# Kernel optimization log

Hardware: AMD Instinct MI355X
Metric: run time of the kernel (lower is better)

The kernel has to match this reference:

```python
import jax, jax.numpy as jnp
import numpy as np

NEG_INF = -1e9  # matches masked_fill value -1000000000.0
SLOPE = 0.2     # LeakyReLU negative slope


def setup_inputs() -> dict:
    key = jax.random.key(0)
    k1, k2, k3, k4 = jax.random.split(key, 4)
    B, N, Fin, Fout = 16, 1024, 256, 256
    h = jax.random.normal(k1, (B, N, Fin), dtype=jnp.float32)
    adj = jax.random.randint(k2, (B, N, N), 0, 2, dtype=jnp.int32)
    W = jax.random.normal(k3, (Fin, Fout), dtype=jnp.float32) * (1.0 / np.sqrt(Fin))
    a = jax.random.normal(k4, (2 * Fout,), dtype=jnp.float32) * (1.0 / np.sqrt(2 * Fout))
    return {"h": h, "adj": adj, "W": W, "a": a}


def reference(h, adj, W, a):
    # h: [B,N,Fin], adj: [B,N,N] (0/1), W: [Fin,Fout], a: [2*Fout]
    Fout = W.shape[1]
    Wh = jnp.einsum("bnf,fo->bno", h, W)            # [B,N,Fout]
    a1, a2 = a[:Fout], a[Fout:]
    # e[b,i,j] = leakyrelu( Wh[b,i]·a1 + Wh[b,j]·a2 )  == a(cat(Wh_i, Wh_j))
    f1 = Wh @ a1                                     # [B,N]
    f2 = Wh @ a2                                     # [B,N]
    e = jax.nn.leaky_relu(f1[:, :, None] + f2[:, None, :], negative_slope=SLOPE)
    e = jnp.where(adj == 0, NEG_INF, e)              # mask non-edges
    attention = jax.nn.softmax(e, axis=-1)           # [B,N,N]
    # dropout is identity at eval / p=0
    h_prime = jnp.einsum("bij,bjo->bio", attention, Wh)  # [B,N,Fout]
    return h_prime
```

## Files before the change

### kernel.cpp

```cpp
#include <hip/hip_runtime.h>

typedef __attribute__((ext_vector_type(8))) short bf16x8;
typedef __attribute__((ext_vector_type(4))) float f32x4;

__device__ __forceinline__ unsigned short f2bf(float x) {
    unsigned int u = __float_as_uint(x);
    u += 0x7FFFu + ((u >> 16) & 1u);
    return (unsigned short)(u >> 16);
}

__device__ __forceinline__ void gl_lds16(const void* g, void* l) {
    __builtin_amdgcn_global_load_lds(
        (__attribute__((address_space(1))) void*)((void*)g),
        (__attribute__((address_space(3))) void*)l, 16, 0, 0);
}

__global__ __launch_bounds__(256) void prep(const float* __restrict__ W,
                                            short* __restrict__ WbT) {
    __shared__ float tile[32][33];
    const int t = threadIdx.x;
    const int bx = blockIdx.x & 7, by = blockIdx.x >> 3;
    const int r0 = by * 32, c0 = bx * 32;
    const int lr = t >> 5, lc = t & 31;
#pragma unroll
    for (int q = 0; q < 4; ++q)
        tile[q * 8 + lr][lc] = W[(r0 + q * 8 + lr) * 256 + c0 + lc];
    __syncthreads();
#pragma unroll
    for (int q = 0; q < 4; ++q)
        WbT[(c0 + q * 8 + lr) * 256 + r0 + lc] = (short)f2bf(tile[lc][q * 8 + lr]);
}

__global__ __launch_bounds__(256, 4) void wh_f12(const float* __restrict__ h,
                                                 const short* __restrict__ WbT,
                                                 const float* __restrict__ a,
                                                 short* __restrict__ WhT,
                                                 float* __restrict__ f1,
                                                 float* __restrict__ f2) {
    __shared__ short hA[32][264];
    __shared__ float sp[2][4][32];
    const int t = threadIdx.x;
    const int wid = t >> 6, lane = t & 63;
    const int quad = lane >> 4, l15 = lane & 15;
    const int m0 = blockIdx.x * 32;

#pragma unroll
    for (int rr = 0; rr < 2; ++rr) {
        const int r = rr * 16 + (t >> 4), c0 = (t & 15) * 16;
        const float* hp = h + (size_t)(m0 + r) * 256 + c0;
        float4 v0 = *(const float4*)(hp + 0), v1 = *(const float4*)(hp + 4);
        float4 v2 = *(const float4*)(hp + 8), v3 = *(const float4*)(hp + 12);
        bf16x8 w0, w1;
        w0[0] = (short)f2bf(v0.x); w0[1] = (short)f2bf(v0.y);
        w0[2] = (short)f2bf(v0.z); w0[3] = (short)f2bf(v0.w);
        w0[4] = (short)f2bf(v1.x); w0[5] = (short)f2bf(v1.y);
        w0[6] = (short)f2bf(v1.z); w0[7] = (short)f2bf(v1.w);
        w1[0] = (short)f2bf(v2.x); w1[1] = (short)f2bf(v2.y);
        w1[2] = (short)f2bf(v2.z); w1[3] = (short)f2bf(v2.w);
        w1[4] = (short)f2bf(v3.x); w1[5] = (short)f2bf(v3.y);
        w1[6] = (short)f2bf(v3.z); w1[7] = (short)f2bf(v3.w);
        *(bf16x8*)&hA[r][c0] = w0;
        *(bf16x8*)&hA[r][c0 + 8] = w1;
    }
    __syncthreads();

    f32x4 acc[2][4] = {};
#pragma unroll
    for (int kt = 0; kt < 8; ++kt) {
        const int k0 = kt * 32;
        bf16x8 bv[4];
#pragma unroll
        for (int ft = 0; ft < 4; ++ft)
            bv[ft] = *(const bf16x8*)(WbT + (size_t)(wid * 64 + ft * 16 + l15) * 256 + k0 + quad * 8);
        bf16x8 a0 = *(const bf16x8*)&hA[l15][k0 + quad * 8];
        bf16x8 a1 = *(const bf16x8*)&hA[16 + l15][k0 + quad * 8];
#pragma unroll
        for (int ft = 0; ft < 4; ++ft) {
            acc[0][ft] = __builtin_amdgcn_mfma_f32_16x16x32_bf16(a0, bv[ft], acc[0][ft], 0, 0, 0);
            acc[1][ft] = __builtin_amdgcn_mfma_f32_16x16x32_bf16(a1, bv[ft], acc[1][ft], 0, 0, 0);
        }
    }

    const int b = m0 >> 10;
#pragma unroll
    for (int mf = 0; mf < 2; ++mf) {
        const int il0 = (m0 & 1023) + mf * 16 + quad * 4;
#pragma unroll
        for (int ft = 0; ft < 4; ++ft) {
            const int f = wid * 64 + ft * 16 + l15;
            ushort4 pk;
            pk.x = f2bf(acc[mf][ft][0]);
            pk.y = f2bf(acc[mf][ft][1]);
            pk.z = f2bf(acc[mf][ft][2]);
            pk.w = f2bf(acc[mf][ft][3]);
            *(ushort4*)(WhT + ((size_t)b << 18) + (size_t)f * 1024 + il0) = pk;
        }
    }

    float a1v[4], a2v[4];
#pragma unroll
    for (int ft = 0; ft < 4; ++ft) {
        a1v[ft] = a[wid * 64 + ft * 16 + l15];
        a2v[ft] = a[256 + wid * 64 + ft * 16 + l15];
    }
    float p1[2][4] = {}, p2[2][4] = {};
#pragma unroll
    for (int mf = 0; mf < 2; ++mf)
#pragma unroll
        for (int ft = 0; ft < 4; ++ft)
#pragma unroll
            for (int r = 0; r < 4; ++r) {
                p1[mf][r] += acc[mf][ft][r] * a1v[ft];
                p2[mf][r] += acc[mf][ft][r] * a2v[ft];
            }
#pragma unroll
    for (int off = 1; off < 16; off <<= 1)
#pragma unroll
        for (int mf = 0; mf < 2; ++mf)
#pragma unroll
            for (int r = 0; r < 4; ++r) {
                p1[mf][r] += __shfl_xor(p1[mf][r], off);
                p2[mf][r] += __shfl_xor(p2[mf][r], off);
            }
    if (l15 == 0)
#pragma unroll
        for (int mf = 0; mf < 2; ++mf)
#pragma unroll
            for (int r = 0; r < 4; ++r) {
                sp[0][wid][mf * 16 + quad * 4 + r] = p1[mf][r];
                sp[1][wid][mf * 16 + quad * 4 + r] = p2[mf][r];
            }
    __syncthreads();
    if (t < 32) {
        f1[m0 + t] = sp[0][0][t] + sp[0][1][t] + sp[0][2][t] + sp[0][3][t];
        f2[m0 + t] = sp[1][0][t] + sp[1][1][t] + sp[1][2][t] + sp[1][3][t];
    }
}

__global__ __launch_bounds__(256) void stats_p(const int* __restrict__ adj,
                                               const float* __restrict__ f1g,
                                               const float* __restrict__ f2g,
                                               short* __restrict__ P) {
    const int wid = threadIdx.x >> 6, lane = threadIdx.x & 63;
    const int gid = blockIdx.x * 4 + wid;
    const int b = gid >> 10;
    const int* arow = adj + (size_t)gid * 1024;
    const float* f2b = f2g + (b << 10);
    const float f1r = f1g[gid];

    float e[16];
#pragma unroll
    for (int c = 0; c < 4; ++c) {
        int4 av = *(const int4*)(arow + lane * 4 + c * 256);
        float4 fv = *(const float4*)(f2b + lane * 4 + c * 256);
        float x0 = f1r + fv.x, x1 = f1r + fv.y, x2 = f1r + fv.z, x3 = f1r + fv.w;
        e[c * 4 + 0] = av.x ? fmaxf(x0, 0.2f * x0) : -3.0e38f;
        e[c * 4 + 1] = av.y ? fmaxf(x1, 0.2f * x1) : -3.0e38f;
        e[c * 4 + 2] = av.z ? fmaxf(x2, 0.2f * x2) : -3.0e38f;
        e[c * 4 + 3] = av.w ? fmaxf(x3, 0.2f * x3) : -3.0e38f;
    }
    float m = e[0];
#pragma unroll
    for (int q = 1; q < 16; ++q) m = fmaxf(m, e[q]);
#pragma unroll
    for (int off = 32; off; off >>= 1) m = fmaxf(m, __shfl_xor(m, off));

    float p[16];
    float l = 0.f;
#pragma unroll
    for (int q = 0; q < 16; ++q) { p[q] = __expf(e[q] - m); l += p[q]; }
#pragma unroll
    for (int off = 32; off; off >>= 1) l += __shfl_xor(l, off);
    const float invl = 1.0f / l;

    short* prow = P + (size_t)gid * 1024;
#pragma unroll
    for (int c = 0; c < 4; ++c) {
        ushort4 pk;
        pk.x = f2bf(p[c * 4 + 0] * invl);
        pk.y = f2bf(p[c * 4 + 1] * invl);
        pk.z = f2bf(p[c * 4 + 2] * invl);
        pk.w = f2bf(p[c * 4 + 3] * invl);
        *(ushort4*)(prow + lane * 4 + c * 256) = pk;
    }
}

__global__ __launch_bounds__(256, 4) void agg(const short* __restrict__ P,
                                              const short* __restrict__ WhT,
                                              float* __restrict__ out) {
    __shared__ short As[64 * 64];
    __shared__ short Bs[64 * 64];

    const int t = threadIdx.x;
    const int wid = t >> 6, lane = t & 63;
    const int quad = lane >> 4, l15 = lane & 15;
    const int m0 = blockIdx.x * 64, n0 = blockIdx.y * 64, b = blockIdx.z;

    const short* Pb = P + ((size_t)b << 20);
    const short* Wb = WhT + ((size_t)b << 18);

    const int r0 = t >> 3;
    const int w0 = (t & 7) ^ (r0 & 7);
    const short* gaA0 = Pb + (size_t)(m0 + r0) * 1024 + w0 * 8;
    const short* gaA1 = Pb + (size_t)(m0 + 32 + r0) * 1024 + w0 * 8;
    const short* gaB0 = Wb + (size_t)(n0 + r0) * 1024 + w0 * 8;
    const short* gaB1 = Wb + (size_t)(n0 + 32 + r0) * 1024 + w0 * 8;
    short* lA0 = As + t * 8;
    short* lA1 = As + 2048 + t * 8;
    short* lB0 = Bs + t * 8;
    short* lB1 = Bs + 2048 + t * 8;

    f32x4 acc[4] = {};
    const int ra = wid * 16 + l15;

    for (int k0 = 0; k0 < 1024; k0 += 64) {
        gl_lds16(gaA0 + k0, lA0);
        gl_lds16(gaA1 + k0, lA1);
        gl_lds16(gaB0 + k0, lB0);
        gl_lds16(gaB1 + k0, lB1);
        __syncthreads();

#pragma unroll
        for (int kt = 0; kt < 2; ++kt) {
            const int w = kt * 4 + quad;
            bf16x8 av = *(const bf16x8*)(As + ra * 64 + ((w ^ (ra & 7)) * 8));
#pragma unroll
            for (int nf = 0; nf < 4; ++nf) {
                const int rb = nf * 16 + l15;
                bf16x8 bv = *(const bf16x8*)(Bs + rb * 64 + ((w ^ (rb & 7)) * 8));
                acc[nf] = __builtin_amdgcn_mfma_f32_16x16x32_bf16(av, bv, acc[nf], 0, 0, 0);
            }
        }
        __syncthreads();
    }

    const int i = m0 + wid * 16 + quad * 4;
#pragma unroll
    for (int nf = 0; nf < 4; ++nf) {
        float* op = out + (size_t)((b << 10) + i) * 256 + n0 + nf * 16 + l15;
        op[0]   = acc[nf][0];
        op[256] = acc[nf][1];
        op[512] = acc[nf][2];
        op[768] = acc[nf][3];
    }
}

extern "C" void kernel_launch(void* const* d_in, const int* in_sizes, int n_in,
                              void* d_out, int out_size, void* d_ws, size_t ws_size,
                              hipStream_t stream) {
    const float* h   = (const float*)d_in[0];
    const int*   adj = (const int*)d_in[1];
    const float* W   = (const float*)d_in[2];
    const float* a   = (const float*)d_in[3];
    float* out = (float*)d_out;

    short* WbT = (short*)d_ws;
    float* f1  = (float*)(WbT + 65536);
    float* f2  = f1 + 16384;
    short* WhT = (short*)(f2 + 16384);
    short* P   = WhT + 16 * 256 * 1024;

    prep<<<64, 256, 0, stream>>>(W, WbT);
    wh_f12<<<512, 256, 0, stream>>>(h, WbT, a, WhT, f1, f2);
    stats_p<<<4096, 256, 0, stream>>>(adj, f1, f2, P);
    agg<<<dim3(16, 4, 16), 256, 0, stream>>>(P, WhT, out);
}
```

Measured before the change: 152.2 us.

## Widen agg tile to 64x128 with 2x4 MFMA fragments and XCD-aware block mapping

The aggregation GEMM now computes a 64x128 output tile per block instead of 64x64. Each wave computes 32x64 using 2x4 MFMA fragments, which reuses A and B fragments from LDS across more MFMAs. The grid becomes a flat 512 blocks with an index mapping that groups blocks of the same batch onto one XCD, to improve L2 reuse of the P and Wh rows. The cost is more LDS per block and more accumulator registers, and the block count halves, which may reduce occupancy and the number of waves.

```diff
diff --git a/kernel.cpp b/kernel.cpp
--- a/kernel.cpp
+++ b/kernel.cpp
@@ -189,59 +189,83 @@
                                               const short* __restrict__ WhT,
                                               float* __restrict__ out) {
     __shared__ short As[64 * 64];
-    __shared__ short Bs[64 * 64];
+    __shared__ short Bs[128 * 64];
 
     const int t = threadIdx.x;
     const int wid = t >> 6, lane = t & 63;
     const int quad = lane >> 4, l15 = lane & 15;
-    const int m0 = blockIdx.x * 64, n0 = blockIdx.y * 64, b = blockIdx.z;
+
+    const int id = blockIdx.x;
+    const int xcd = id & 7, rest = id >> 3;
+    const int b = xcd + 8 * (rest & 1);
+    const int n0 = ((rest >> 1) & 1) * 128;
+    const int m0 = (rest >> 2) * 64;
 
     const short* Pb = P + ((size_t)b << 20);
     const short* Wb = WhT + ((size_t)b << 18);
 
-    const int r0 = t >> 3;
-    const int w0 = (t & 7) ^ (r0 & 7);
-    const short* gaA0 = Pb + (size_t)(m0 + r0) * 1024 + w0 * 8;
-    const short* gaA1 = Pb + (size_t)(m0 + 32 + r0) * 1024 + w0 * 8;
-    const short* gaB0 = Wb + (size_t)(n0 + r0) * 1024 + w0 * 8;
-    const short* gaB1 = Wb + (size_t)(n0 + 32 + r0) * 1024 + w0 * 8;
+    const int rA = t >> 3, wA = (t & 7) ^ (rA & 7);
+    const short* gA0 = Pb + (size_t)(m0 + rA) * 1024 + wA * 8;
+    const short* gA1 = Pb + (size_t)(m0 + 32 + rA) * 1024 + wA * 8;
+    const short* gB0 = Wb + (size_t)(n0 + rA) * 1024 + wA * 8;
+    const short* gB1 = Wb + (size_t)(n0 + 32 + rA) * 1024 + wA * 8;
+    const short* gB2 = Wb + (size_t)(n0 + 64 + rA) * 1024 + wA * 8;
+    const short* gB3 = Wb + (size_t)(n0 + 96 + rA) * 1024 + wA * 8;
     short* lA0 = As + t * 8;
     short* lA1 = As + 2048 + t * 8;
     short* lB0 = Bs + t * 8;
     short* lB1 = Bs + 2048 + t * 8;
-
-    f32x4 acc[4] = {};
-    const int ra = wid * 16 + l15;
+    short* lB2 = Bs + 4096 + t * 8;
+    short* lB3 = Bs + 6144 + t * 8;
+
+    const int mh = (wid & 1) * 32;
+    const int nq = (wid >> 1) * 64;
+
+    f32x4 acc[2][4] = {};
 
     for (int k0 = 0; k0 < 1024; k0 += 64) {
-        gl_lds16(gaA0 + k0, lA0);
-        gl_lds16(gaA1 + k0, lA1);
-        gl_lds16(gaB0 + k0, lB0);
-        gl_lds16(gaB1 + k0, lB1);
+        gl_lds16(gA0 + k0, lA0);
+        gl_lds16(gA1 + k0, lA1);
+        gl_lds16(gB0 + k0, lB0);
+        gl_lds16(gB1 + k0, lB1);
+        gl_lds16(gB2 + k0, lB2);
+        gl_lds16(gB3 + k0, lB3);
         __syncthreads();
 
 #pragma unroll
         for (int kt = 0; kt < 2; ++kt) {
             const int w = kt * 4 + quad;
-            bf16x8 av = *(const bf16x8*)(As + ra * 64 + ((w ^ (ra & 7)) * 8));
+            bf16x8 av[2], bv[4];
+#pragma unroll
+            for (int mf = 0; mf < 2; ++mf) {
+                const int r = mh + mf * 16 + l15;
+                av[mf] = *(const bf16x8*)(As + r * 64 + ((w ^ (r & 7)) * 8));
+            }
 #pragma unroll
             for (int nf = 0; nf < 4; ++nf) {
-                const int rb = nf * 16 + l15;
-                bf16x8 bv = *(const bf16x8*)(Bs + rb * 64 + ((w ^ (rb & 7)) * 8));
-                acc[nf] = __builtin_amdgcn_mfma_f32_16x16x32_bf16(av, bv, acc[nf], 0, 0, 0);
-            }
+                const int r = nq + nf * 16 + l15;
+                bv[nf] = *(const bf16x8*)(Bs + r * 64 + ((w ^ (r & 7)) * 8));
+            }
+#pragma unroll
+            for (int mf = 0; mf < 2; ++mf)
+#pragma unroll
+                for (int nf = 0; nf < 4; ++nf)
+                    acc[mf][nf] = __builtin_amdgcn_mfma_f32_16x16x32_bf16(av[mf], bv[nf], acc[mf][nf], 0, 0, 0);
         }
         __syncthreads();
     }
 
-    const int i = m0 + wid * 16 + quad * 4;
-#pragma unroll
-    for (int nf = 0; nf < 4; ++nf) {
-        float* op = out + (size_t)((b << 10) + i) * 256 + n0 + nf * 16 + l15;
-        op[0]   = acc[nf][0];
-        op[256] = acc[nf][1];
-        op[512] = acc[nf][2];
-        op[768] = acc[nf][3];
+#pragma unroll
+    for (int mf = 0; mf < 2; ++mf) {
+        const int i = m0 + mh + mf * 16 + quad * 4;
+#pragma unroll
+        for (int nf = 0; nf < 4; ++nf) {
+            float* op = out + (size_t)((b << 10) + i) * 256 + n0 + nq + nf * 16 + l15;
+            op[0]   = acc[mf][nf][0];
+            op[256] = acc[mf][nf][1];
+            op[512] = acc[mf][nf][2];
+            op[768] = acc[mf][nf][3];
+        }
     }
 }
 
@@ -263,5 +287,5 @@
     prep<<<64, 256, 0, stream>>>(W, WbT);
     wh_f12<<<512, 256, 0, stream>>>(h, WbT, a, WhT, f1, f2);
     stats_p<<<4096, 256, 0, stream>>>(adj, f1, f2, P);
-    agg<<<dim3(16, 4, 16), 256, 0, stream>>>(P, WhT, out);
-}
+    agg<<<512, 256, 0, stream>>>(P, WhT, out);
+}
```

Result: no change. 152.2 us, median of 2 (-0.0%).
